# Performance work log

Measured on AMD Instinct MI355X. Metric: run time of the kernel, lower is better.

The kernel has to match this reference:

```python
import jax, jax.numpy as jnp
import numpy as np


def setup_inputs() -> dict:
    key = jax.random.key(0)
    ks = jax.random.split(key, 5)
    B, S, C, H = 32, 512, 320, 512
    scale = 1.0 / np.sqrt(H)
    return {
        "x": jax.random.normal(ks[0], (B, S, C), dtype=jnp.float32),
        "w_ih": jax.random.normal(ks[1], (4 * H, S), dtype=jnp.float32) * scale,
        "w_hh": jax.random.normal(ks[2], (4 * H, H), dtype=jnp.float32) * scale,
        "b_ih": jax.random.normal(ks[3], (4 * H,), dtype=jnp.float32) * scale,
        "b_hh": jax.random.normal(ks[4], (4 * H,), dtype=jnp.float32) * scale,
    }


def reference(x, w_ih, w_hh, b_ih, b_hh):
    # x: (B, S, C). Original permutes to (B, C, S) and runs a length-1 LSTM per
    # channel with zero initial state -> single LSTM cell step:
    #   gates = x_c @ W_ih^T + b_ih + b_hh   (W_hh @ h0 == 0)
    # PyTorch gate order: i, f, g, o.
    B, S, C = x.shape
    H = w_hh.shape[1]
    gates = jnp.einsum("bsc,gs->bcg", x, w_ih) + b_ih + b_hh  # (B, C, 4H)
    i_g, f_g, g_g, o_g = jnp.split(gates, 4, axis=-1)
    c = jax.nn.sigmoid(i_g) * jnp.tanh(g_g)           # c0 = 0
    h = jax.nn.sigmoid(o_g) * jnp.tanh(c)             # (B, C, H)
    # Faithful to torch: cat over channels along batch dim -> (C*B, H),
    # then reshape to (B, C, H) (scrambles batch/channel order).
    h = jnp.transpose(h, (1, 0, 2)).reshape(B, C, H)
    # dropout is identity in eval mode
    return jnp.transpose(h, (0, 2, 1))                # (B, H, C)
```

## Files before the change

kernel.cpp:

```cpp
#include <hip/hip_runtime.h>
#include <stdint.h>

#define B_  32
#define S_  512
#define C_  320
#define H_  512
#define NROW (B_*C_)

typedef __attribute__((ext_vector_type(8))) short short8;
typedef __attribute__((ext_vector_type(4))) float f32x4;

__device__ __forceinline__ unsigned short f2bf(float x){
  unsigned u = __builtin_bit_cast(unsigned, x);
  u = u + 0x7FFFu + ((u >> 16) & 1u);
  return (unsigned short)(u >> 16);
}
__device__ __forceinline__ float sigf(float x){ return 1.0f/(1.0f + __expf(-x)); }
__device__ __forceinline__ float tanh_fast(float x){ return 2.0f/(1.0f + __expf(-2.0f*x)) - 1.0f; }

__device__ __forceinline__ void gload16(const void* g, void* l){
  __builtin_amdgcn_global_load_lds((const __attribute__((address_space(1))) void*)g,
                                   (__attribute__((address_space(3))) void*)l, 16, 0, 0);
}

__global__ __launch_bounds__(256) void k_prep(const float* __restrict__ w,
                                              const float* __restrict__ x,
                                              unsigned short* __restrict__ aws,
                                              unsigned short* __restrict__ xws){
  const int bidg = blockIdx.x;
  const int tid = threadIdx.x;
  if (bidg < 768){
    int flat = bidg*256 + tid;
    int plane = flat >> 16;
    int rem   = flat & 65535;
    int srow  = (plane == 0 ? 0 : (plane == 1 ? 1024 : 1536));
    float4 v = ((const float4*)w)[srow*128 + rem];
    uint2 p;
    p.x = (unsigned)f2bf(v.x) | ((unsigned)f2bf(v.y) << 16);
    p.y = (unsigned)f2bf(v.z) | ((unsigned)f2bf(v.w) << 16);
    ((uint2*)aws)[flat] = p;
    return;
  }
  __shared__ float lds[64][65];
  const int idx = bidg - 768;
  const int st = idx & 7;
  const int r5 = idx >> 3;
  const int ctt = r5 % 5, b = r5 / 5;
  const int s0 = st*64, c0 = ctt*64;
  const int row = tid >> 2, q = tid & 3;

  const float* src = x + ((size_t)(b*S_ + s0 + row))*C_ + c0 + q*16;
  #pragma unroll
  for (int j = 0; j < 4; j++){
    float4 v = ((const float4*)src)[j];
    lds[row][q*16 + j*4 + 0] = v.x;
    lds[row][q*16 + j*4 + 1] = v.y;
    lds[row][q*16 + j*4 + 2] = v.z;
    lds[row][q*16 + j*4 + 3] = v.w;
  }
  __syncthreads();
  const int crow = row;
  const size_t nprime = (size_t)(c0 + crow)*32 + (size_t)b;
  #pragma unroll
  for (int j = 0; j < 2; j++){
    short8 o;
    #pragma unroll
    for (int e = 0; e < 8; e++)
      o[e] = (short)f2bf(lds[q*16 + j*8 + e][crow]);
    *(short8*)(xws + nprime*S_ + s0 + q*16 + j*8) = o;
  }
}

__global__ __launch_bounds__(256, 4) void k_gemm(const unsigned short* __restrict__ aws,
                                                 const unsigned short* __restrict__ xws,
                                                 const float* __restrict__ b_ih,
                                                 const float* __restrict__ b_hh,
                                                 float* __restrict__ out){
  __shared__ alignas(16) char lds[40960];

  const int tid  = threadIdx.x;
  const int w    = tid >> 6;
  const int lane = tid & 63;
  const int wm = w >> 1, wn = w & 1;

  const int bid = blockIdx.x;
  const int x8 = bid & 7, y = bid >> 3;
  const int kt = y & 7, n2 = y >> 3;
  const int nt = n2*8 + x8;
  const int k0 = kt*64;
  const int nbase = nt*128;

  f32x4 acc[3][2][4];
  #pragma unroll
  for (int gi = 0; gi < 3; gi++)
    #pragma unroll
    for (int mf = 0; mf < 2; mf++)
      #pragma unroll
      for (int nf = 0; nf < 4; nf++)
        acc[gi][mf][nf] = (f32x4){0.f, 0.f, 0.f, 0.f};

  const int cr   = lane >> 3;
  const int slot = ((lane & 7) ^ cr) << 4;

  const char* wsb = (const char*)aws;
  unsigned srcoff[10];
  int      dstoff[10];
  #pragma unroll
  for (int i = 0; i < 10; i++){
    int q = w*10 + i;
    if (q < 24){
      int gi = q >> 3, q8 = q & 7;
      int grow = gi*512 + k0 + q8*8 + cr;
      srcoff[i] = (unsigned)(grow*1024 + slot);
      dstoff[i] = gi*8192 + q8*1024;
    } else {
      int q8 = q - 24;
      int xrow = nbase + q8*8 + cr;
      srcoff[i] = (unsigned)(2097152 + xrow*1024 + slot);
      dstoff[i] = 24576 + q8*1024;
    }
  }

  const int lo16 = (lane >> 4) << 4;
  const int swz  = (lane & 7) << 4;
  const int l15  = lane & 15;

  for (int t = 0; t < 8; t++){
    #pragma unroll
    for (int i = 0; i < 10; i++){
      gload16(wsb + (size_t)srcoff[i], &lds[0] + dstoff[i]);
      srcoff[i] += 128;
    }
    __syncthreads();
    #pragma unroll
    for (int ks = 0; ks < 2; ks++){
      const int colb = (ks*64 + lo16) ^ swz;
      short8 aF[3][2], bF[4];
      #pragma unroll
      for (int gi = 0; gi < 3; gi++)
        #pragma unroll
        for (int mf = 0; mf < 2; mf++)
          aF[gi][mf] = *(const short8*)(&lds[0] + gi*8192 + (wm*32 + mf*16 + l15)*128 + colb);
      #pragma unroll
      for (int nf = 0; nf < 4; nf++)
        bF[nf] = *(const short8*)(&lds[0] + 24576 + (wn*64 + nf*16 + l15)*128 + colb);
      #pragma unroll
      for (int gi = 0; gi < 3; gi++)
        #pragma unroll
        for (int mf = 0; mf < 2; mf++)
          #pragma unroll
          for (int nf = 0; nf < 4; nf++)
            acc[gi][mf][nf] = __builtin_amdgcn_mfma_f32_16x16x32_bf16(aF[gi][mf], bF[nf], acc[gi][mf][nf], 0, 0, 0);
    }
    __syncthreads();
  }

  float* tr = (float*)&lds[0];
  #pragma unroll
  for (int mf = 0; mf < 2; mf++){
    const int kl = wm*32 + mf*16 + ((lane >> 4) << 2);
    const int kg = k0 + kl;
    float bi[4], bg[4], bo[4];
    #pragma unroll
    for (int r = 0; r < 4; r++){
      bi[r] = b_ih[kg + r]        + b_hh[kg + r];
      bg[r] = b_ih[1024 + kg + r] + b_hh[1024 + kg + r];
      bo[r] = b_ih[1536 + kg + r] + b_hh[1536 + kg + r];
    }
    #pragma unroll
    for (int nf = 0; nf < 4; nf++){
      const int nl = wn*64 + nf*16 + l15;
      float4 hv;
      float h[4];
      #pragma unroll
      for (int r = 0; r < 4; r++){
        float iv = acc[0][mf][nf][r] + bi[r];
        float gv = acc[1][mf][nf][r] + bg[r];
        float ov = acc[2][mf][nf][r] + bo[r];
        float ce = sigf(iv) * tanh_fast(gv);
        h[r] = sigf(ov) * tanh_fast(ce);
      }
      hv.x = h[0]; hv.y = h[1]; hv.z = h[2]; hv.w = h[3];
      *(float4*)(tr + nl*68 + kl) = hv;
    }
  }
  __syncthreads();

  const int ko  = tid >> 2;
  const int sub = tid & 3;
  const size_t krow_off = (size_t)(k0 + ko)*C_;
  #pragma unroll
  for (int jj = 0; jj < 8; jj++){
    const int nl = sub*32 + jj*4;
    const int ng = nbase + nl;
    const int b2 = ng / 320;
    const int c2 = ng - b2*320;
    float4 v;
    v.x = tr[(nl+0)*68 + ko];
    v.y = tr[(nl+1)*68 + ko];
    v.z = tr[(nl+2)*68 + ko];
    v.w = tr[(nl+3)*68 + ko];
    *(float4*)(out + (size_t)b2*(H_*C_) + krow_off + c2) = v;
  }
}

extern "C" void kernel_launch(void* const* d_in, const int* in_sizes, int n_in,
                              void* d_out, int out_size, void* d_ws, size_t ws_size,
                              hipStream_t stream){
  const float* x    = (const float*)d_in[0];
  const float* w_ih = (const float*)d_in[1];
  const float* b_ih = (const float*)d_in[3];
  const float* b_hh = (const float*)d_in[4];
  float* out = (float*)d_out;

  char* ws = (char*)d_ws;
  unsigned short* aws = (unsigned short*)(ws);
  unsigned short* xws = (unsigned short*)(ws + 2097152);

  k_prep <<<2048, 256, 0, stream>>>(w_ih, x, aws, xws);
  k_gemm <<<640, 256, 0, stream>>>(aws, xws, b_ih, b_hh, out);
}
```

Measured before the change: 54.89 us.

## Load full-K tiles into large LDS with smaller output tiles and more blocks

The GEMM kernel now loads the entire K=512 slice of both operands into 160KB of LDS in a single step and then runs 16 MFMA k-steps with no intermediate barriers. The output tile shrinks from 64x128 to 32x64 and the grid grows from 640 to 2560 blocks. The goal is to remove the per-iteration load/sync pipeline and spread work over more blocks, but the large LDS footprint allows only one block per CU and leaves no overlap between loads and compute. The prep transpose store and the epilogue store indexing are also rearranged for better coalescing.

```diff
diff --git a/kernel.cpp b/kernel.cpp
--- a/kernel.cpp
+++ b/kernel.cpp
@@ -5,7 +5,6 @@
 #define S_  512
 #define C_  320
 #define H_  512
-#define NROW (B_*C_)
 
 typedef __attribute__((ext_vector_type(8))) short short8;
 typedef __attribute__((ext_vector_type(4))) float f32x4;
@@ -59,24 +58,26 @@
     lds[row][q*16 + j*4 + 3] = v.w;
   }
   __syncthreads();
-  const int crow = row;
-  const size_t nprime = (size_t)(c0 + crow)*32 + (size_t)b;
-  #pragma unroll
-  for (int j = 0; j < 2; j++){
+  const int wr2 = tid >> 3;
+  const int l8  = tid & 7;
+  #pragma unroll
+  for (int half = 0; half < 2; half++){
+    const int crow = half*32 + wr2;
+    const size_t nprime = (size_t)(c0 + crow)*32 + (size_t)b;
     short8 o;
     #pragma unroll
     for (int e = 0; e < 8; e++)
-      o[e] = (short)f2bf(lds[q*16 + j*8 + e][crow]);
-    *(short8*)(xws + nprime*S_ + s0 + q*16 + j*8) = o;
-  }
-}
-
-__global__ __launch_bounds__(256, 4) void k_gemm(const unsigned short* __restrict__ aws,
-                                                 const unsigned short* __restrict__ xws,
-                                                 const float* __restrict__ b_ih,
-                                                 const float* __restrict__ b_hh,
-                                                 float* __restrict__ out){
-  __shared__ alignas(16) char lds[40960];
+      o[e] = (short)f2bf(lds[l8*8 + e][crow]);
+    *(short8*)(xws + nprime*S_ + s0 + l8*8) = o;
+  }
+}
+
+__global__ __launch_bounds__(256) void k_gemm(const unsigned short* __restrict__ aws,
+                                              const unsigned short* __restrict__ xws,
+                                              const float* __restrict__ b_ih,
+                                              const float* __restrict__ b_hh,
+                                              float* __restrict__ out){
+  __shared__ alignas(16) char lds[163840];
 
   const int tid  = threadIdx.x;
   const int w    = tid >> 6;
@@ -85,81 +86,66 @@
 
   const int bid = blockIdx.x;
   const int x8 = bid & 7, y = bid >> 3;
-  const int kt = y & 7, n2 = y >> 3;
-  const int nt = n2*8 + x8;
-  const int k0 = kt*64;
-  const int nbase = nt*128;
-
-  f32x4 acc[3][2][4];
+  const int mt = y & 15, g = y >> 4;
+  const int nt = g*8 + x8;
+  const int k0 = mt*32;
+  const int nbase = nt*64;
+
+  f32x4 acc[3][2];
   #pragma unroll
   for (int gi = 0; gi < 3; gi++)
     #pragma unroll
-    for (int mf = 0; mf < 2; mf++)
+    for (int nf = 0; nf < 2; nf++)
+      acc[gi][nf] = (f32x4){0.f, 0.f, 0.f, 0.f};
+
+  const char* wsb = (const char*)aws;
+  {
+    #pragma unroll
+    for (int i = 0; i < 24; i++){
+      const int q = i*4 + w;
+      const int gi = q >> 5, row = q & 31;
+      const int slot = (lane << 4) ^ ((row & 7) << 4);
+      const unsigned src = (unsigned)((gi*512 + k0 + row)*1024) + (unsigned)slot;
+      gload16(wsb + (size_t)src, &lds[0] + gi*32768 + row*1024);
+    }
+    #pragma unroll
+    for (int i = 0; i < 16; i++){
+      const int row = i*4 + w;
+      const int slot = (lane << 4) ^ ((row & 7) << 4);
+      const unsigned src = 2097152u + (unsigned)((nbase + row)*1024) + (unsigned)slot;
+      gload16(wsb + (size_t)src, &lds[0] + 98304 + row*1024);
+    }
+  }
+  __syncthreads();
+
+  const int l15  = lane & 15;
+  const int hi16 = (lane >> 4) << 4;
+  const int xkey = (l15 & 7) << 4;
+  const int arow = wm*16 + l15;
+  const int brow0 = wn*32 + l15;
+
+  #pragma unroll
+  for (int ks = 0; ks < 16; ks++){
+    const int colb = (ks*64 + hi16) ^ xkey;
+    short8 aF[3], bF[2];
+    #pragma unroll
+    for (int gi = 0; gi < 3; gi++)
+      aF[gi] = *(const short8*)(&lds[0] + gi*32768 + arow*1024 + colb);
+    #pragma unroll
+    for (int nf = 0; nf < 2; nf++)
+      bF[nf] = *(const short8*)(&lds[0] + 98304 + (brow0 + nf*16)*1024 + colb);
+    #pragma unroll
+    for (int gi = 0; gi < 3; gi++)
       #pragma unroll
-      for (int nf = 0; nf < 4; nf++)
-        acc[gi][mf][nf] = (f32x4){0.f, 0.f, 0.f, 0.f};
-
-  const int cr   = lane >> 3;
-  const int slot = ((lane & 7) ^ cr) << 4;
-
-  const char* wsb = (const char*)aws;
-  unsigned srcoff[10];
-  int      dstoff[10];
-  #pragma unroll
-  for (int i = 0; i < 10; i++){
-    int q = w*10 + i;
-    if (q < 24){
-      int gi = q >> 3, q8 = q & 7;
-      int grow = gi*512 + k0 + q8*8 + cr;
-      srcoff[i] = (unsigned)(grow*1024 + slot);
-      dstoff[i] = gi*8192 + q8*1024;
-    } else {
-      int q8 = q - 24;
-      int xrow = nbase + q8*8 + cr;
-      srcoff[i] = (unsigned)(2097152 + xrow*1024 + slot);
-      dstoff[i] = 24576 + q8*1024;
-    }
-  }
-
-  const int lo16 = (lane >> 4) << 4;
-  const int swz  = (lane & 7) << 4;
-  const int l15  = lane & 15;
-
-  for (int t = 0; t < 8; t++){
-    #pragma unroll
-    for (int i = 0; i < 10; i++){
-      gload16(wsb + (size_t)srcoff[i], &lds[0] + dstoff[i]);
-      srcoff[i] += 128;
-    }
-    __syncthreads();
-    #pragma unroll
-    for (int ks = 0; ks < 2; ks++){
-      const int colb = (ks*64 + lo16) ^ swz;
-      short8 aF[3][2], bF[4];
-      #pragma unroll
-      for (int gi = 0; gi < 3; gi++)
-        #pragma unroll
-        for (int mf = 0; mf < 2; mf++)
-          aF[gi][mf] = *(const short8*)(&lds[0] + gi*8192 + (wm*32 + mf*16 + l15)*128 + colb);
-      #pragma unroll
-      for (int nf = 0; nf < 4; nf++)
-        bF[nf] = *(const short8*)(&lds[0] + 24576 + (wn*64 + nf*16 + l15)*128 + colb);
-      #pragma unroll
-      for (int gi = 0; gi < 3; gi++)
-        #pragma unroll
-        for (int mf = 0; mf < 2; mf++)
-          #pragma unroll
-          for (int nf = 0; nf < 4; nf++)
-            acc[gi][mf][nf] = __builtin_amdgcn_mfma_f32_16x16x32_bf16(aF[gi][mf], bF[nf], acc[gi][mf][nf], 0, 0, 0);
-    }
-    __syncthreads();
-  }
+      for (int nf = 0; nf < 2; nf++)
+        acc[gi][nf] = __builtin_amdgcn_mfma_f32_16x16x32_bf16(aF[gi], bF[nf], acc[gi][nf], 0, 0, 0);
+  }
+  __syncthreads();
 
   float* tr = (float*)&lds[0];
-  #pragma unroll
-  for (int mf = 0; mf < 2; mf++){
-    const int kl = wm*32 + mf*16 + ((lane >> 4) << 2);
-    const int kg = k0 + kl;
+  {
+    const int kbl = wm*16 + ((lane >> 4) << 2);
+    const int kg  = k0 + kbl;
     float bi[4], bg[4], bo[4];
     #pragma unroll
     for (int r = 0; r < 4; r++){
@@ -168,39 +154,35 @@
       bo[r] = b_ih[1536 + kg + r] + b_hh[1536 + kg + r];
     }
     #pragma unroll
-    for (int nf = 0; nf < 4; nf++){
-      const int nl = wn*64 + nf*16 + l15;
-      float4 hv;
-      float h[4];
+    for (int nf = 0; nf < 2; nf++){
+      const int nl = wn*32 + nf*16 + l15;
       #pragma unroll
       for (int r = 0; r < 4; r++){
-        float iv = acc[0][mf][nf][r] + bi[r];
-        float gv = acc[1][mf][nf][r] + bg[r];
-        float ov = acc[2][mf][nf][r] + bo[r];
+        float iv = acc[0][nf][r] + bi[r];
+        float gv = acc[1][nf][r] + bg[r];
+        float ov = acc[2][nf][r] + bo[r];
         float ce = sigf(iv) * tanh_fast(gv);
-        h[r] = sigf(ov) * tanh_fast(ce);
+        tr[(kbl + r)*68 + nl] = sigf(ov) * tanh_fast(ce);
       }
-      hv.x = h[0]; hv.y = h[1]; hv.z = h[2]; hv.w = h[3];
-      *(float4*)(tr + nl*68 + kl) = hv;
-    }
-  }
-  __syncthreads();
-
-  const int ko  = tid >> 2;
-  const int sub = tid & 3;
-  const size_t krow_off = (size_t)(k0 + ko)*C_;
-  #pragma unroll
-  for (int jj = 0; jj < 8; jj++){
-    const int nl = sub*32 + jj*4;
-    const int ng = nbase + nl;
-    const int b2 = ng / 320;
-    const int c2 = ng - b2*320;
+    }
+  }
+  __syncthreads();
+
+  const int klo   = tid >> 3;
+  const int lane8 = tid & 7;
+  const size_t rowoff = (size_t)(k0 + klo)*C_;
+  #pragma unroll
+  for (int j = 0; j < 2; j++){
+    const int nl0 = j*32 + lane8*4;
+    const int ng  = nbase + nl0;
+    const int b2  = ng / 320;
+    const int c2  = ng - b2*320;
     float4 v;
-    v.x = tr[(nl+0)*68 + ko];
-    v.y = tr[(nl+1)*68 + ko];
-    v.z = tr[(nl+2)*68 + ko];
-    v.w = tr[(nl+3)*68 + ko];
-    *(float4*)(out + (size_t)b2*(H_*C_) + krow_off + c2) = v;
+    v.x = tr[klo*68 + nl0 + 0];
+    v.y = tr[klo*68 + nl0 + 1];
+    v.z = tr[klo*68 + nl0 + 2];
+    v.w = tr[klo*68 + nl0 + 3];
+    *(float4*)(out + (size_t)b2*(H_*C_) + rowoff + c2) = v;
   }
 }
 
@@ -218,5 +200,5 @@
   unsigned short* xws = (unsigned short*)(ws + 2097152);
 
   k_prep <<<2048, 256, 0, stream>>>(w_ih, x, aws, xws);
-  k_gemm <<<640, 256, 0, stream>>>(aws, xws, b_ih, b_hh, out);
-}
+  k_gemm <<<2560, 256, 0, stream>>>(aws, xws, b_ih, b_hh, out);
+}
```

Result: slower. 58.82 us (+7.2%).
